# Performance work log

Measured on AMD Instinct MI355X. Metric: run time of the kernel, lower is better.

## Reference

```python
import jax, jax.numpy as jnp
import numpy as np

C = 1024          # columns
K = 16            # cells per column
S = 32            # distal segments per cell
Y = 128           # synapses per segment
N = C * K         # num cells
PERM_THR = 0.5
ACT_THR = 10
LR = 0.1          # volatile learning rate
MOD = 1.0         # modulation_signal


def setup_inputs() -> dict:
    key = jax.random.key(0)
    k1, k2, k3, k4, k5 = jax.random.split(key, 5)
    x = jax.random.uniform(k1, (C,)) < 0.03                      # sparse column SDR
    prev_active_cells = jax.random.uniform(k2, (N,)) < 0.12      # prev-step active cells
    distal_connections = jax.random.randint(k3, (N, S, Y), 0, N, dtype=jnp.int32)
    volatile_permanences = jax.random.uniform(k4, (N, S, Y), dtype=jnp.float32)
    consolidated_permanences = jax.random.uniform(k5, (N, S, Y), dtype=jnp.float32) * 0.6
    return {
        "x": x,
        "prev_active_cells": prev_active_cells,
        "distal_connections": distal_connections,
        "volatile_permanences": volatile_permanences,
        "consolidated_permanences": consolidated_permanences,
    }


def reference(x, prev_active_cells, distal_connections, volatile_permanences, consolidated_permanences):
    conn = jnp.clip(distal_connections, 0, N - 1)                # [N,S,Y]
    x_active = x.astype(bool)                                    # [C]
    prev_any = prev_active_cells.any()

    # ---- phase 1: predictive state per column from prev_active_cells ----
    presyn_prev = prev_active_cells[conn]                        # [N,S,Y] irregular gather
    connected = (volatile_permanences > PERM_THR) | (consolidated_permanences > PERM_THR)
    active_syn = (connected & presyn_prev).sum(-1)               # [N,S]
    pred_cell = (active_syn >= ACT_THR).any(-1)                  # [N]
    pred_col = pred_cell.reshape(C, K)                           # [C,K]
    col_predicted = pred_col.any(-1)                             # [C]

    # ---- burst winner selection (unthresholded overlaps, argmax over K*S) ----
    overlaps = presyn_prev.sum(-1).astype(jnp.int32)             # [N,S]
    best_flat = jnp.argmax(overlaps.reshape(C, K * S), axis=-1)  # [C]
    burst_winner_local = best_flat // S                          # [C] (== 0 when no prev activity, matching torch fallback)
    burst_winner_mask = jax.nn.one_hot(burst_winner_local, K, dtype=bool)  # [C,K]

    winner = jnp.where(col_predicted[:, None], pred_col, burst_winner_mask)  # [C,K]
    winner = winner & x_active[:, None]                          # only active columns

    # new active cells: only bursting columns set cells (predicted columns set none, per source)
    new_active = jnp.broadcast_to((x_active & ~col_predicted)[:, None], (C, K))
    new_active_flat = new_active.reshape(-1)                     # [N]

    # ---- learning: update volatile permanences on each winner cell's best segment ----
    best_seg = jnp.argmax(overlaps, axis=-1)                     # [N]
    rows = jnp.arange(N)
    presyn_best = presyn_prev[rows, best_seg]                    # [N,Y]
    old_row = volatile_permanences[rows, best_seg]               # [N,Y]
    pot = LR * MOD
    pun = pot * 0.1
    new_row = jnp.clip(old_row + jnp.where(presyn_best, pot, -pun), 0.0, 1.0)
    learn_mask = winner.reshape(-1) & prev_any                   # [N] (torch skips learning if no prev activity)
    vol_new = volatile_permanences.at[rows, best_seg].set(
        jnp.where(learn_mask[:, None], new_row, old_row))

    # ---- phase 2: predictive state for next step from new active cells + updated perms ----
    presyn_new = new_active_flat[conn]                           # [N,S,Y]
    connected2 = (vol_new > PERM_THR) | (consolidated_permanences > PERM_THR)
    pred_next = (((connected2 & presyn_new).sum(-1)) >= ACT_THR).any(-1)  # [N]

    num_active = x_active.sum()
    num_pred = (x_active & col_predicted).sum()
    acc = jnp.where(num_active > 0,
                    num_pred.astype(jnp.float32) / jnp.maximum(num_active, 1).astype(jnp.float32),
                    jnp.float32(1.0))
    return new_active_flat, pred_next, acc
```

## Files before the change

kernel.cpp:

```cpp
#include <hip/hip_runtime.h>
#include <stdint.h>

#define C_ 1024
#define K_ 16
#define S_ 32
#define Y_ 128
#define N_ (C_ * K_)
#define ACT_THR 10
#define PERM_THR 0.5f
#define POT 0.1f
#define PUN 0.01f

#define WS_NUM_ACTIVE 0
#define WS_NUM_PRED   1
#define WS_NBURST     2
#define WS_LEARN_CNT  3
#define WS_PREV_ANY   4
#define WS_BURSTMASK  8
#define WS_PREVMASK   64
#define WS_CELLINFO   1024
#define WS_LIST       (1024 + N_)

__global__ __launch_bounds__(256) void pack_kernel(const int* __restrict__ prev,
                                                   unsigned* __restrict__ ws) {
    const int tid = threadIdx.x;
    if (tid < 64) ws[tid] = 0u;
    __syncthreads();
    bool any = false;
    for (int w = tid; w < 512; w += 256) {
        unsigned m = 0u;
        #pragma unroll
        for (int b = 0; b < 32; ++b) {
            if (prev[w * 32 + b] != 0) m |= (1u << b);
        }
        ws[WS_PREVMASK + w] = m;
        any |= (m != 0u);
    }
    if (any) atomicOr(&ws[WS_PREV_ANY], 1u);
}

__global__ __launch_bounds__(256) void phase1_kernel(const int*   __restrict__ conn,
                                                     const float* __restrict__ vol,
                                                     const float* __restrict__ cons,
                                                     unsigned*    __restrict__ ws) {
    __shared__ unsigned prevmask[512];
    __shared__ int sA[S_];
    __shared__ int sO[S_];
    const int tid = threadIdx.x;
    for (int i = tid; i < 512; i += 256) prevmask[i] = ws[WS_PREVMASK + i];
    __syncthreads();

    const int cell = blockIdx.x;
    const int wave = tid >> 6;
    const int lane = tid & 63;
    const int half = lane >> 5;
    const int l32  = lane & 31;
    const int sh   = half * 32;

    #pragma unroll
    for (int t = 0; t < 4; ++t) {
        const int seg = wave * 8 + t * 2 + half;
        const size_t base = ((size_t)cell * S_ + seg) * Y_ + (size_t)(l32 * 4);
        const int4   cv = *reinterpret_cast<const int4*>(conn + base);
        const float4 vv = *reinterpret_cast<const float4*>(vol + base);
        const float4 sv = *reinterpret_cast<const float4*>(cons + base);

        const int m0 = min(max(cv.x, 0), N_ - 1);
        const int m1 = min(max(cv.y, 0), N_ - 1);
        const int m2 = min(max(cv.z, 0), N_ - 1);
        const int m3 = min(max(cv.w, 0), N_ - 1);
        const bool p0 = (prevmask[m0 >> 5] >> (m0 & 31)) & 1u;
        const bool p1 = (prevmask[m1 >> 5] >> (m1 & 31)) & 1u;
        const bool p2 = (prevmask[m2 >> 5] >> (m2 & 31)) & 1u;
        const bool p3 = (prevmask[m3 >> 5] >> (m3 & 31)) & 1u;
        const bool c0 = (vv.x > PERM_THR) || (sv.x > PERM_THR);
        const bool c1 = (vv.y > PERM_THR) || (sv.y > PERM_THR);
        const bool c2 = (vv.z > PERM_THR) || (sv.z > PERM_THR);
        const bool c3 = (vv.w > PERM_THR) || (sv.w > PERM_THR);

        const uint64_t bp0 = __ballot(p0), bp1 = __ballot(p1),
                       bp2 = __ballot(p2), bp3 = __ballot(p3);
        const uint64_t ba0 = __ballot(p0 && c0), ba1 = __ballot(p1 && c1),
                       ba2 = __ballot(p2 && c2), ba3 = __ballot(p3 && c3);

        const int ov = __popc((unsigned)(bp0 >> sh)) + __popc((unsigned)(bp1 >> sh)) +
                       __popc((unsigned)(bp2 >> sh)) + __popc((unsigned)(bp3 >> sh));
        const int ac = __popc((unsigned)(ba0 >> sh)) + __popc((unsigned)(ba1 >> sh)) +
                       __popc((unsigned)(ba2 >> sh)) + __popc((unsigned)(ba3 >> sh));
        if (l32 == 0) { sO[seg] = ov; sA[seg] = ac; }
    }
    __syncthreads();
    if (tid == 0) {
        bool pred = false;
        int bo = -1, bs = 0;
        #pragma unroll
        for (int s = 0; s < S_; ++s) {
            pred |= (sA[s] >= ACT_THR);
            if (sO[s] > bo) { bo = sO[s]; bs = s; }
        }
        ws[WS_CELLINFO + cell] = (pred ? 1u : 0u) | ((unsigned)bs << 8) | ((unsigned)bo << 16);
    }
}

__global__ __launch_bounds__(256) void column_kernel(const int* __restrict__ x,
                                                     unsigned*  __restrict__ ws,
                                                     float*     __restrict__ out_new_active) {
    const int c = blockIdx.x * 256 + threadIdx.x;
    if (c >= C_) return;
    const bool xa = (x[c] != 0);
    const int base = c * K_;

    unsigned info[K_];
    bool colpred = false;
    int bo = -1, bk = 0;
    #pragma unroll
    for (int k = 0; k < K_; ++k) {
        const unsigned inf = ws[WS_CELLINFO + base + k];
        info[k] = inf;
        if (inf & 1u) colpred = true;
        const int ov = (int)((inf >> 16) & 0xFFu);
        if (ov > bo) { bo = ov; bk = k; }
    }

    const bool burst = xa && !colpred;
    const float nav = burst ? 1.0f : 0.0f;
    #pragma unroll
    for (int k = 0; k < K_; ++k) out_new_active[base + k] = nav;

    if (xa) {
        atomicAdd(&ws[WS_NUM_ACTIVE], 1u);
        if (colpred) atomicAdd(&ws[WS_NUM_PRED], 1u);
    }
    if (burst) {
        atomicAdd(&ws[WS_NBURST], 1u);
        atomicOr(&ws[WS_BURSTMASK + (c >> 5)], 1u << (c & 31));
    }
    if (xa) {
        if (colpred) {
            #pragma unroll
            for (int k = 0; k < K_; ++k) {
                if (info[k] & 1u) {
                    const unsigned i = atomicAdd(&ws[WS_LEARN_CNT], 1u);
                    ws[WS_LIST + i] = (unsigned)(base + k);
                }
            }
        } else {
            const unsigned i = atomicAdd(&ws[WS_LEARN_CNT], 1u);
            ws[WS_LIST + i] = (unsigned)(base + bk);
        }
    }
}

__global__ __launch_bounds__(256) void learn_kernel(const int* __restrict__ conn,
                                                    float*     __restrict__ vol,
                                                    unsigned*  __restrict__ ws,
                                                    float*     __restrict__ out_acc) {
    __shared__ unsigned prevmask[512];
    const int tid = threadIdx.x;
    for (int i = tid; i < 512; i += 256) prevmask[i] = ws[WS_PREVMASK + i];
    __syncthreads();

    if (blockIdx.x == 0 && tid == 0) {
        const int na  = (int)ws[WS_NUM_ACTIVE];
        const int np_ = (int)ws[WS_NUM_PRED];
        out_acc[0] = (na > 0) ? ((float)np_ / (float)na) : 1.0f;
    }
    if (ws[WS_PREV_ANY] == 0u) return;

    const int cnt    = (int)ws[WS_LEARN_CNT];
    const int wave   = (blockIdx.x * 256 + tid) >> 6;
    const int lane   = tid & 63;
    const int nwaves = gridDim.x * 4;

    for (int e = wave; e < cnt; e += nwaves) {
        const int cell = (int)ws[WS_LIST + e];
        const int seg  = (int)((ws[WS_CELLINFO + cell] >> 8) & 0xFFu);
        const size_t base = ((size_t)cell * S_ + seg) * Y_ + (size_t)(lane * 2);
        const int2 cv = *reinterpret_cast<const int2*>(conn + base);
        float2 vv = *reinterpret_cast<const float2*>(vol + base);
        const int m0 = min(max(cv.x, 0), N_ - 1);
        const int m1 = min(max(cv.y, 0), N_ - 1);
        const bool p0 = (prevmask[m0 >> 5] >> (m0 & 31)) & 1u;
        const bool p1 = (prevmask[m1 >> 5] >> (m1 & 31)) & 1u;
        vv.x = fminf(fmaxf(vv.x + (p0 ? POT : -PUN), 0.0f), 1.0f);
        vv.y = fminf(fmaxf(vv.y + (p1 ? POT : -PUN), 0.0f), 1.0f);
        *reinterpret_cast<float2*>(vol + base) = vv;
    }
}

__global__ __launch_bounds__(256) void phase2_kernel(const int*   __restrict__ conn,
                                                     const float* __restrict__ vol,
                                                     const float* __restrict__ cons,
                                                     const unsigned* __restrict__ ws,
                                                     float* __restrict__ out_pred_next) {
    const int cell = blockIdx.x;
    const int tid  = threadIdx.x;
    if (ws[WS_NBURST] == 0u) {
        if (tid == 0) out_pred_next[cell] = 0.0f;
        return;
    }
    __shared__ unsigned burstmask[32];
    __shared__ int sA[S_];
    if (tid < 32) burstmask[tid] = ws[WS_BURSTMASK + tid];
    __syncthreads();

    const int wave = tid >> 6;
    const int lane = tid & 63;
    const int half = lane >> 5;
    const int l32  = lane & 31;
    const int sh   = half * 32;

    #pragma unroll
    for (int t = 0; t < 4; ++t) {
        const int seg = wave * 8 + t * 2 + half;
        const size_t base = ((size_t)cell * S_ + seg) * Y_ + (size_t)(l32 * 4);
        const int4   cv = *reinterpret_cast<const int4*>(conn + base);
        const float4 vv = *reinterpret_cast<const float4*>(vol + base);
        const float4 sv = *reinterpret_cast<const float4*>(cons + base);

        const int m0 = min(max(cv.x, 0), N_ - 1) >> 4;
        const int m1 = min(max(cv.y, 0), N_ - 1) >> 4;
        const int m2 = min(max(cv.z, 0), N_ - 1) >> 4;
        const int m3 = min(max(cv.w, 0), N_ - 1) >> 4;
        const bool p0 = (burstmask[m0 >> 5] >> (m0 & 31)) & 1u;
        const bool p1 = (burstmask[m1 >> 5] >> (m1 & 31)) & 1u;
        const bool p2 = (burstmask[m2 >> 5] >> (m2 & 31)) & 1u;
        const bool p3 = (burstmask[m3 >> 5] >> (m3 & 31)) & 1u;
        const bool c0 = (vv.x > PERM_THR) || (sv.x > PERM_THR);
        const bool c1 = (vv.y > PERM_THR) || (sv.y > PERM_THR);
        const bool c2 = (vv.z > PERM_THR) || (sv.z > PERM_THR);
        const bool c3 = (vv.w > PERM_THR) || (sv.w > PERM_THR);

        const uint64_t ba0 = __ballot(p0 && c0), ba1 = __ballot(p1 && c1),
                       ba2 = __ballot(p2 && c2), ba3 = __ballot(p3 && c3);
        const int ac = __popc((unsigned)(ba0 >> sh)) + __popc((unsigned)(ba1 >> sh)) +
                       __popc((unsigned)(ba2 >> sh)) + __popc((unsigned)(ba3 >> sh));
        if (l32 == 0) sA[seg] = ac;
    }
    __syncthreads();
    if (tid == 0) {
        bool pred = false;
        #pragma unroll
        for (int s = 0; s < S_; ++s) pred |= (sA[s] >= ACT_THR);
        out_pred_next[cell] = pred ? 1.0f : 0.0f;
    }
}

extern "C" void kernel_launch(void* const* d_in, const int* in_sizes, int n_in,
                              void* d_out, int out_size, void* d_ws, size_t ws_size,
                              hipStream_t stream) {
    const int*   x    = (const int*)d_in[0];
    const int*   prev = (const int*)d_in[1];
    const int*   conn = (const int*)d_in[2];
    float*       vol  = (float*)d_in[3];
    const float* cons = (const float*)d_in[4];
    float*    out = (float*)d_out;
    unsigned* ws  = (unsigned*)d_ws;

    pack_kernel  <<<1,    256, 0, stream>>>(prev, ws);
    phase1_kernel<<<N_,   256, 0, stream>>>(conn, vol, cons, ws);
    column_kernel<<<C_/256, 256, 0, stream>>>(x, ws, out);
    learn_kernel <<<64,   256, 0, stream>>>(conn, vol, ws, out + 2 * N_);
    phase2_kernel<<<N_,   256, 0, stream>>>(conn, vol, cons, ws, out + N_);
}
```

Measured before the change: 670.7 us.

## Map one cell per wave with software prefetch in phase kernels

Phase1 and phase2 now assign one cell per wavefront (8 cells per block, 2048 blocks), so a single wave loops over all 32 segments instead of a whole 256-thread block handling one cell. Each iteration prefetches the next segment's loads, and the block-wide shared-memory reductions and syncthreads are replaced by wave-level shuffle/any reductions with a packed max key for the argmax. The pack kernel also moves to 512 threads using vectorized int4 loads and a ballot. The goal is to cut block launch and sync overhead and keep more loads in flight on this bandwidth-bound workload, at the cost of more registers per thread and fewer total waves.

```diff
diff --git a/kernel.cpp b/kernel.cpp
--- a/kernel.cpp
+++ b/kernel.cpp
@@ -21,22 +21,26 @@
 #define WS_CELLINFO   1024
 #define WS_LIST       (1024 + N_)
 
-__global__ __launch_bounds__(256) void pack_kernel(const int* __restrict__ prev,
+#define P1_BLOCKS 2048
+
+__global__ __launch_bounds__(512) void pack_kernel(const int* __restrict__ prev,
                                                    unsigned* __restrict__ ws) {
     const int tid = threadIdx.x;
     if (tid < 64) ws[tid] = 0u;
     __syncthreads();
-    bool any = false;
-    for (int w = tid; w < 512; w += 256) {
-        unsigned m = 0u;
-        #pragma unroll
-        for (int b = 0; b < 32; ++b) {
-            if (prev[w * 32 + b] != 0) m |= (1u << b);
-        }
-        ws[WS_PREVMASK + w] = m;
-        any |= (m != 0u);
-    }
-    if (any) atomicOr(&ws[WS_PREV_ANY], 1u);
+    const int4* p = reinterpret_cast<const int4*>(prev + tid * 32);
+    unsigned m = 0u;
+    #pragma unroll
+    for (int q = 0; q < 8; ++q) {
+        const int4 v = p[q];
+        m |= (v.x != 0 ? 1u : 0u) << (q * 4 + 0);
+        m |= (v.y != 0 ? 1u : 0u) << (q * 4 + 1);
+        m |= (v.z != 0 ? 1u : 0u) << (q * 4 + 2);
+        m |= (v.w != 0 ? 1u : 0u) << (q * 4 + 3);
+    }
+    ws[WS_PREVMASK + tid] = m;
+    const bool any = (__ballot(m != 0u) != 0ull);
+    if ((tid & 63) == 0 && any) atomicOr(&ws[WS_PREV_ANY], 1u);
 }
 
 __global__ __launch_bounds__(256) void phase1_kernel(const int*   __restrict__ conn,
@@ -44,61 +48,78 @@
                                                      const float* __restrict__ cons,
                                                      unsigned*    __restrict__ ws) {
     __shared__ unsigned prevmask[512];
-    __shared__ int sA[S_];
-    __shared__ int sO[S_];
     const int tid = threadIdx.x;
     for (int i = tid; i < 512; i += 256) prevmask[i] = ws[WS_PREVMASK + i];
     __syncthreads();
 
-    const int cell = blockIdx.x;
     const int wave = tid >> 6;
     const int lane = tid & 63;
     const int half = lane >> 5;
     const int l32  = lane & 31;
     const int sh   = half * 32;
 
-    #pragma unroll
-    for (int t = 0; t < 4; ++t) {
-        const int seg = wave * 8 + t * 2 + half;
-        const size_t base = ((size_t)cell * S_ + seg) * Y_ + (size_t)(l32 * 4);
-        const int4   cv = *reinterpret_cast<const int4*>(conn + base);
-        const float4 vv = *reinterpret_cast<const float4*>(vol + base);
-        const float4 sv = *reinterpret_cast<const float4*>(cons + base);
-
-        const int m0 = min(max(cv.x, 0), N_ - 1);
-        const int m1 = min(max(cv.y, 0), N_ - 1);
-        const int m2 = min(max(cv.z, 0), N_ - 1);
-        const int m3 = min(max(cv.w, 0), N_ - 1);
-        const bool p0 = (prevmask[m0 >> 5] >> (m0 & 31)) & 1u;
-        const bool p1 = (prevmask[m1 >> 5] >> (m1 & 31)) & 1u;
-        const bool p2 = (prevmask[m2 >> 5] >> (m2 & 31)) & 1u;
-        const bool p3 = (prevmask[m3 >> 5] >> (m3 & 31)) & 1u;
-        const bool c0 = (vv.x > PERM_THR) || (sv.x > PERM_THR);
-        const bool c1 = (vv.y > PERM_THR) || (sv.y > PERM_THR);
-        const bool c2 = (vv.z > PERM_THR) || (sv.z > PERM_THR);
-        const bool c3 = (vv.w > PERM_THR) || (sv.w > PERM_THR);
-
-        const uint64_t bp0 = __ballot(p0), bp1 = __ballot(p1),
-                       bp2 = __ballot(p2), bp3 = __ballot(p3);
-        const uint64_t ba0 = __ballot(p0 && c0), ba1 = __ballot(p1 && c1),
-                       ba2 = __ballot(p2 && c2), ba3 = __ballot(p3 && c3);
-
-        const int ov = __popc((unsigned)(bp0 >> sh)) + __popc((unsigned)(bp1 >> sh)) +
-                       __popc((unsigned)(bp2 >> sh)) + __popc((unsigned)(bp3 >> sh));
-        const int ac = __popc((unsigned)(ba0 >> sh)) + __popc((unsigned)(ba1 >> sh)) +
-                       __popc((unsigned)(ba2 >> sh)) + __popc((unsigned)(ba3 >> sh));
-        if (l32 == 0) { sO[seg] = ov; sA[seg] = ac; }
-    }
-    __syncthreads();
-    if (tid == 0) {
-        bool pred = false;
-        int bo = -1, bs = 0;
-        #pragma unroll
-        for (int s = 0; s < S_; ++s) {
-            pred |= (sA[s] >= ACT_THR);
-            if (sO[s] > bo) { bo = sO[s]; bs = s; }
+    #pragma unroll 1
+    for (int ci = 0; ci < 2; ++ci) {
+        const int cell = blockIdx.x * 8 + wave + ci * 4;
+        const size_t cellbase = (size_t)cell * (S_ * Y_) + (size_t)(l32 * 4);
+
+        size_t a = cellbase + (size_t)half * Y_;
+        int4   cv_n = *reinterpret_cast<const int4*>(conn + a);
+        float4 vv_n = *reinterpret_cast<const float4*>(vol + a);
+        float4 sv_n = *reinterpret_cast<const float4*>(cons + a);
+
+        unsigned key = 0u;
+        bool predf = false;
+
+        #pragma unroll 2
+        for (int i = 0; i < 16; ++i) {
+            const int4   cv = cv_n;
+            const float4 vv = vv_n;
+            const float4 sv = sv_n;
+            if (i < 15) {
+                const size_t nb = cellbase + (size_t)(2 * (i + 1) + half) * Y_;
+                cv_n = *reinterpret_cast<const int4*>(conn + nb);
+                vv_n = *reinterpret_cast<const float4*>(vol + nb);
+                sv_n = *reinterpret_cast<const float4*>(cons + nb);
+            }
+
+            const int m0 = min(max(cv.x, 0), N_ - 1);
+            const int m1 = min(max(cv.y, 0), N_ - 1);
+            const int m2 = min(max(cv.z, 0), N_ - 1);
+            const int m3 = min(max(cv.w, 0), N_ - 1);
+            const bool p0 = (prevmask[m0 >> 5] >> (m0 & 31)) & 1u;
+            const bool p1 = (prevmask[m1 >> 5] >> (m1 & 31)) & 1u;
+            const bool p2 = (prevmask[m2 >> 5] >> (m2 & 31)) & 1u;
+            const bool p3 = (prevmask[m3 >> 5] >> (m3 & 31)) & 1u;
+            const bool c0 = (vv.x > PERM_THR) || (sv.x > PERM_THR);
+            const bool c1 = (vv.y > PERM_THR) || (sv.y > PERM_THR);
+            const bool c2 = (vv.z > PERM_THR) || (sv.z > PERM_THR);
+            const bool c3 = (vv.w > PERM_THR) || (sv.w > PERM_THR);
+
+            const uint64_t bp0 = __ballot(p0), bp1 = __ballot(p1),
+                           bp2 = __ballot(p2), bp3 = __ballot(p3);
+            const uint64_t ba0 = __ballot(p0 && c0), ba1 = __ballot(p1 && c1),
+                           ba2 = __ballot(p2 && c2), ba3 = __ballot(p3 && c3);
+
+            const int ov = __popc((unsigned)(bp0 >> sh)) + __popc((unsigned)(bp1 >> sh)) +
+                           __popc((unsigned)(bp2 >> sh)) + __popc((unsigned)(bp3 >> sh));
+            const int ac = __popc((unsigned)(ba0 >> sh)) + __popc((unsigned)(ba1 >> sh)) +
+                           __popc((unsigned)(ba2 >> sh)) + __popc((unsigned)(ba3 >> sh));
+
+            predf |= (ac >= ACT_THR);
+            const int seg = 2 * i + half;
+            const unsigned k2 = ((unsigned)ov << 6) | (unsigned)(63 - seg);
+            key = max(key, k2);
         }
-        ws[WS_CELLINFO + cell] = (pred ? 1u : 0u) | ((unsigned)bs << 8) | ((unsigned)bo << 16);
+
+        const unsigned okey = (unsigned)__shfl_xor((int)key, 32);
+        const unsigned fkey = max(key, okey);
+        const bool fpred = (__any(predf ? 1 : 0) != 0);
+        if (lane == 0) {
+            const int bo = (int)(fkey >> 6);
+            const int bs = 63 - (int)(fkey & 63u);
+            ws[WS_CELLINFO + cell] = (fpred ? 1u : 0u) | ((unsigned)bs << 8) | ((unsigned)bo << 16);
+        }
     }
 }
 
@@ -193,16 +214,18 @@
                                                      const float* __restrict__ cons,
                                                      const unsigned* __restrict__ ws,
                                                      float* __restrict__ out_pred_next) {
-    const int cell = blockIdx.x;
-    const int tid  = threadIdx.x;
-    if (ws[WS_NBURST] == 0u) {
-        if (tid == 0) out_pred_next[cell] = 0.0f;
+    __shared__ unsigned nburst_s;
+    __shared__ unsigned burstmask[32];
+    const int tid = threadIdx.x;
+    if (tid == 0) nburst_s = ws[WS_NBURST];
+    if (tid >= 64 && tid < 96) burstmask[tid - 64] = ws[WS_BURSTMASK + (tid - 64)];
+    __syncthreads();
+
+    const int cbase = blockIdx.x * 8;
+    if (nburst_s == 0u) {
+        if (tid < 8) out_pred_next[cbase + tid] = 0.0f;
         return;
     }
-    __shared__ unsigned burstmask[32];
-    __shared__ int sA[S_];
-    if (tid < 32) burstmask[tid] = ws[WS_BURSTMASK + tid];
-    __syncthreads();
 
     const int wave = tid >> 6;
     const int lane = tid & 63;
@@ -210,39 +233,52 @@
     const int l32  = lane & 31;
     const int sh   = half * 32;
 
-    #pragma unroll
-    for (int t = 0; t < 4; ++t) {
-        const int seg = wave * 8 + t * 2 + half;
-        const size_t base = ((size_t)cell * S_ + seg) * Y_ + (size_t)(l32 * 4);
-        const int4   cv = *reinterpret_cast<const int4*>(conn + base);
-        const float4 vv = *reinterpret_cast<const float4*>(vol + base);
-        const float4 sv = *reinterpret_cast<const float4*>(cons + base);
-
-        const int m0 = min(max(cv.x, 0), N_ - 1) >> 4;
-        const int m1 = min(max(cv.y, 0), N_ - 1) >> 4;
-        const int m2 = min(max(cv.z, 0), N_ - 1) >> 4;
-        const int m3 = min(max(cv.w, 0), N_ - 1) >> 4;
-        const bool p0 = (burstmask[m0 >> 5] >> (m0 & 31)) & 1u;
-        const bool p1 = (burstmask[m1 >> 5] >> (m1 & 31)) & 1u;
-        const bool p2 = (burstmask[m2 >> 5] >> (m2 & 31)) & 1u;
-        const bool p3 = (burstmask[m3 >> 5] >> (m3 & 31)) & 1u;
-        const bool c0 = (vv.x > PERM_THR) || (sv.x > PERM_THR);
-        const bool c1 = (vv.y > PERM_THR) || (sv.y > PERM_THR);
-        const bool c2 = (vv.z > PERM_THR) || (sv.z > PERM_THR);
-        const bool c3 = (vv.w > PERM_THR) || (sv.w > PERM_THR);
-
-        const uint64_t ba0 = __ballot(p0 && c0), ba1 = __ballot(p1 && c1),
-                       ba2 = __ballot(p2 && c2), ba3 = __ballot(p3 && c3);
-        const int ac = __popc((unsigned)(ba0 >> sh)) + __popc((unsigned)(ba1 >> sh)) +
-                       __popc((unsigned)(ba2 >> sh)) + __popc((unsigned)(ba3 >> sh));
-        if (l32 == 0) sA[seg] = ac;
-    }
-    __syncthreads();
-    if (tid == 0) {
-        bool pred = false;
-        #pragma unroll
-        for (int s = 0; s < S_; ++s) pred |= (sA[s] >= ACT_THR);
-        out_pred_next[cell] = pred ? 1.0f : 0.0f;
+    #pragma unroll 1
+    for (int ci = 0; ci < 2; ++ci) {
+        const int cell = cbase + wave + ci * 4;
+        const size_t cellbase = (size_t)cell * (S_ * Y_) + (size_t)(l32 * 4);
+
+        size_t a = cellbase + (size_t)half * Y_;
+        int4   cv_n = *reinterpret_cast<const int4*>(conn + a);
+        float4 vv_n = *reinterpret_cast<const float4*>(vol + a);
+        float4 sv_n = *reinterpret_cast<const float4*>(cons + a);
+
+        bool predf = false;
+
+        #pragma unroll 2
+        for (int i = 0; i < 16; ++i) {
+            const int4   cv = cv_n;
+            const float4 vv = vv_n;
+            const float4 sv = sv_n;
+            if (i < 15) {
+                const size_t nb = cellbase + (size_t)(2 * (i + 1) + half) * Y_;
+                cv_n = *reinterpret_cast<const int4*>(conn + nb);
+                vv_n = *reinterpret_cast<const float4*>(vol + nb);
+                sv_n = *reinterpret_cast<const float4*>(cons + nb);
+            }
+
+            const int m0 = min(max(cv.x, 0), N_ - 1) >> 4;
+            const int m1 = min(max(cv.y, 0), N_ - 1) >> 4;
+            const int m2 = min(max(cv.z, 0), N_ - 1) >> 4;
+            const int m3 = min(max(cv.w, 0), N_ - 1) >> 4;
+            const bool p0 = (burstmask[m0 >> 5] >> (m0 & 31)) & 1u;
+            const bool p1 = (burstmask[m1 >> 5] >> (m1 & 31)) & 1u;
+            const bool p2 = (burstmask[m2 >> 5] >> (m2 & 31)) & 1u;
+            const bool p3 = (burstmask[m3 >> 5] >> (m3 & 31)) & 1u;
+            const bool c0 = (vv.x > PERM_THR) || (sv.x > PERM_THR);
+            const bool c1 = (vv.y > PERM_THR) || (sv.y > PERM_THR);
+            const bool c2 = (vv.z > PERM_THR) || (sv.z > PERM_THR);
+            const bool c3 = (vv.w > PERM_THR) || (sv.w > PERM_THR);
+
+            const uint64_t ba0 = __ballot(p0 && c0), ba1 = __ballot(p1 && c1),
+                           ba2 = __ballot(p2 && c2), ba3 = __ballot(p3 && c3);
+            const int ac = __popc((unsigned)(ba0 >> sh)) + __popc((unsigned)(ba1 >> sh)) +
+                           __popc((unsigned)(ba2 >> sh)) + __popc((unsigned)(ba3 >> sh));
+            predf |= (ac >= ACT_THR);
+        }
+
+        const bool fpred = (__any(predf ? 1 : 0) != 0);
+        if (lane == 0) out_pred_next[cell] = fpred ? 1.0f : 0.0f;
     }
 }
 
@@ -257,9 +293,9 @@
     float*    out = (float*)d_out;
     unsigned* ws  = (unsigned*)d_ws;
 
-    pack_kernel  <<<1,    256, 0, stream>>>(prev, ws);
-    phase1_kernel<<<N_,   256, 0, stream>>>(conn, vol, cons, ws);
-    column_kernel<<<C_/256, 256, 0, stream>>>(x, ws, out);
-    learn_kernel <<<64,   256, 0, stream>>>(conn, vol, ws, out + 2 * N_);
-    phase2_kernel<<<N_,   256, 0, stream>>>(conn, vol, cons, ws, out + N_);
-}
+    pack_kernel  <<<1,        512, 0, stream>>>(prev, ws);
+    phase1_kernel<<<P1_BLOCKS, 256, 0, stream>>>(conn, vol, cons, ws);
+    column_kernel<<<C_ / 256,  256, 0, stream>>>(x, ws, out);
+    learn_kernel <<<64,        256, 0, stream>>>(conn, vol, ws, out + 2 * N_);
+    phase2_kernel<<<P1_BLOCKS, 256, 0, stream>>>(conn, vol, cons, ws, out + N_);
+}
```

After: 670.4 us. No clear change (-0.0%).
